# Kernel optimization log

Hardware: AMD Instinct MI355X
Metric: run time of the kernel (lower is better)

## Reference

```python
import jax, jax.numpy as jnp
import numpy as np

H = 8  # heads
EPS = 1e-5


def adaln(x, t, W, b):
    # AdaLayerNorm: emb = Linear(t); scale, shift = chunk(emb, 2, dim=-1)
    emb = t @ W + b                      # [B,1,2*D]
    scale, shift = jnp.split(emb, 2, axis=-1)
    mu = jnp.mean(x, axis=-1, keepdims=True)
    var = jnp.var(x, axis=-1, keepdims=True)
    xn = (x - mu) / jnp.sqrt(var + EPS)  # elementwise_affine=False
    return xn * (1.0 + scale) + shift


def attention(x, ctx, Wq, Wk, Wv, Wo, bo):
    B, N, D = x.shape
    d = D // H
    q = (x @ Wq).reshape(B, N, H, d).transpose(0, 2, 1, 3)          # [B,H,N,d]
    k = (ctx @ Wk).reshape(B, ctx.shape[1], H, d).transpose(0, 2, 1, 3)
    v = (ctx @ Wv).reshape(B, ctx.shape[1], H, d).transpose(0, 2, 1, 3)
    sim = jnp.einsum('bhid,bhjd->bhij', q, k) * (d ** -0.5)
    attn = jax.nn.softmax(sim, axis=-1)
    out = jnp.einsum('bhij,bhjd->bhid', attn, v)
    out = out.transpose(0, 2, 1, 3).reshape(B, N, D)
    return out @ Wo + bo


def geglu_ff(x, W1, b1, W2, b2):
    u, g = jnp.split(x @ W1 + b1, 2, axis=-1)
    return (u * jax.nn.gelu(g, approximate=False)) @ W2 + b2


def setup_inputs() -> dict:
    key = jax.random.key(0)
    ks = jax.random.split(key, 16)
    D = 512
    s = 0.02
    inp = {
        'x': jax.random.normal(ks[0], (2, 2048, D), jnp.float32),
        't': jax.random.normal(ks[1], (2, 1, D), jnp.float32),
        'cond': jax.random.normal(ks[2], (2, 1024, D), jnp.float32),
        'n1_w': jax.random.normal(ks[3], (D, 2 * D), jnp.float32) * s,
        'n1_b': jnp.zeros((2 * D,), jnp.float32),
        'n2_w': jax.random.normal(ks[4], (D, 2 * D), jnp.float32) * s,
        'n2_b': jnp.zeros((2 * D,), jnp.float32),
        'n4_w': jax.random.normal(ks[5], (D, 2 * D), jnp.float32) * s,
        'n4_b': jnp.zeros((2 * D,), jnp.float32),
        'a1_q': jax.random.normal(ks[6], (D, D), jnp.float32) * s,
        'a1_k': jax.random.normal(ks[7], (D, D), jnp.float32) * s,
        'a1_v': jax.random.normal(ks[8], (D, D), jnp.float32) * s,
        'a1_o': jax.random.normal(ks[9], (D, D), jnp.float32) * s,
        'a1_ob': jnp.zeros((D,), jnp.float32),
        'a2_q': jax.random.normal(ks[10], (D, D), jnp.float32) * s,
        'a2_k': jax.random.normal(ks[11], (D, D), jnp.float32) * s,
        'a2_v': jax.random.normal(ks[12], (D, D), jnp.float32) * s,
        'a2_o': jax.random.normal(ks[13], (D, D), jnp.float32) * s,
        'a2_ob': jnp.zeros((D,), jnp.float32),
        'ff_w1': jax.random.normal(ks[14], (D, 8 * D), jnp.float32) * s,
        'ff_b1': jnp.zeros((8 * D,), jnp.float32),
        'ff_w2': jax.random.normal(ks[15], (4 * D, D), jnp.float32) * s,
        'ff_b2': jnp.zeros((D,), jnp.float32),
    }
    return inp


def reference(x, t, cond, n1_w, n1_b, n2_w, n2_b, n4_w, n4_b,
              a1_q, a1_k, a1_v, a1_o, a1_ob,
              a2_q, a2_k, a2_v, a2_o, a2_ob,
              ff_w1, ff_b1, ff_w2, ff_b2):
    # BasicTransformerBlock, is_deform=False, withT=False, inference (dropout/droppath = identity, LayerScale = identity since init_values=0)
    h = adaln(x, t, n1_w, n1_b)
    x = attention(h, h, a1_q, a1_k, a1_v, a1_o, a1_ob) + x
    h = adaln(x, t, n2_w, n2_b)
    x = attention(h, cond, a2_q, a2_k, a2_v, a2_o, a2_ob) + x
    h = adaln(x, t, n4_w, n4_b)
    x = geglu_ff(h, ff_w1, ff_b1, ff_w2, ff_b2) + x
    return x
```

## Files before the change

### kernel.cpp

```cpp
#include <hip/hip_runtime.h>
#include <math.h>

#define D_MODEL 512
#define NHEADS  8
#define DHEAD   64

typedef __bf16  bf16x2 __attribute__((ext_vector_type(2)));
typedef __bf16  bf16x4 __attribute__((ext_vector_type(4)));
typedef __bf16  bf16x8 __attribute__((ext_vector_type(8)));
typedef float   f32x4  __attribute__((ext_vector_type(4)));

#define QSCALE 0.18033688f
#define DEFER_THR 11.5416f

__device__ __forceinline__ void gload16(const __bf16* g, __bf16* l) {
    __builtin_amdgcn_global_load_lds(
        (const __attribute__((address_space(1))) unsigned int*)g,
        (__attribute__((address_space(3))) unsigned int*)l, 16, 0, 0);
}

__device__ __forceinline__ void transpose_tile(
        const float* __restrict__ src, __bf16* __restrict__ dst,
        int K, int N, int k0, int n0) {
    __shared__ float t[64][65];
    int tid = threadIdx.x;
    int r = tid >> 6, c = tid & 63;
#pragma unroll
    for (int i = 0; i < 16; ++i)
        t[r + 4 * i][c] = src[(size_t)(k0 + r + 4 * i) * N + n0 + c];
    __syncthreads();
#pragma unroll
    for (int i = 0; i < 16; ++i)
        dst[(size_t)(n0 + r + 4 * i) * K + k0 + c] = (__bf16)t[c][r + 4 * i];
}

struct PrepArgs {
    const float *t, *n1w, *n1b, *n2w, *n2b, *n4w, *n4b;
    float* emb;
    const float* ws[8]; __bf16* wd[8];
    const float *ffw1, *ffw2;
    __bf16 *ff1t, *ff2t;
    const float* cond; __bf16* cbf;
    int B, condN;
};

__global__ __launch_bounds__(256) void prep_kernel(PrepArgs a) {
    int bb = blockIdx.x, tid = threadIdx.x;
    if (bb < 24) {
        int gI = bb * 256 + tid;
        int per = a.B * 2 * D_MODEL;
        if (gI >= 3 * per) return;
        int norm = gI / per;
        int rem  = gI - norm * per;
        int b = rem / (2 * D_MODEL);
        int c = rem % (2 * D_MODEL);
        const float* W  = (norm == 0) ? a.n1w : (norm == 1 ? a.n2w : a.n4w);
        const float* bb_= (norm == 0) ? a.n1b : (norm == 1 ? a.n2b : a.n4b);
        const float* trow = a.t + (size_t)b * D_MODEL;
        float acc = bb_[c];
        for (int k = 0; k < D_MODEL; ++k)
            acc = fmaf(trow[k], W[(size_t)k * (2 * D_MODEL) + c], acc);
        a.emb[gI] = acc;
    } else if (bb < 536) {
        int w = (bb - 24) >> 6, tI = (bb - 24) & 63;
        transpose_tile(a.ws[w], a.wd[w], 512, 512, (tI >> 3) << 6, (tI & 7) << 6);
    } else if (bb < 1048) {
        int tI = bb - 536;
        transpose_tile(a.ffw1, a.ff1t, 512, 4096, (tI & 7) << 6, (tI >> 3) << 6);
    } else if (bb < 1304) {
        int tI = bb - 1048;
        transpose_tile(a.ffw2, a.ff2t, 2048, 512, (tI >> 3) << 6, (tI & 7) << 6);
    } else {
        int i = ((bb - 1304) * 256 + tid) * 4;
        if (i >= a.condN) return;
        float4 v = *(const float4*)(a.cond + i);
        bf16x2 p0, p1;
        p0[0] = (__bf16)v.x; p0[1] = (__bf16)v.y;
        p1[0] = (__bf16)v.z; p1[1] = (__bf16)v.w;
        *(bf16x2*)(a.cbf + i)     = p0;
        *(bf16x2*)(a.cbf + i + 2) = p1;
    }
}

__global__ __launch_bounds__(256) void adaln_apply_kernel(
        const float* __restrict__ x, const float* __restrict__ emb_n,
        __bf16* __restrict__ h, int N) {
    int row = blockIdx.x;
    int b = row / N;
    const float* xr = x + (size_t)row * D_MODEL;
    int tid = threadIdx.x;
    float2 v = *(const float2*)(xr + 2 * tid);
    float s = v.x + v.y, sq = v.x * v.x + v.y * v.y;
#pragma unroll
    for (int off = 32; off; off >>= 1) {
        s  += __shfl_xor(s, off);
        sq += __shfl_xor(sq, off);
    }
    __shared__ float rs[4], rq[4];
    if ((tid & 63) == 0) { rs[tid >> 6] = s; rq[tid >> 6] = sq; }
    __syncthreads();
    float tot  = rs[0] + rs[1] + rs[2] + rs[3];
    float totq = rq[0] + rq[1] + rq[2] + rq[3];
    float mu  = tot * (1.0f / D_MODEL);
    float var = totq * (1.0f / D_MODEL) - mu * mu;
    float inv = rsqrtf(var + 1e-5f);
    const float* er = emb_n + (size_t)b * (2 * D_MODEL);
    float2 sc = *(const float2*)(er + 2 * tid);
    float2 sh = *(const float2*)(er + D_MODEL + 2 * tid);
    bf16x2 o;
    o[0] = (__bf16)((v.x - mu) * inv * (1.0f + sc.x) + sh.x);
    o[1] = (__bf16)((v.y - mu) * inv * (1.0f + sc.y) + sh.y);
    *(bf16x2*)(h + (size_t)row * D_MODEL + 2 * tid) = o;
}

template<int OUT, int WM>
__device__ __forceinline__ void gemm_body(
        const __bf16* __restrict__ A, const __bf16* __restrict__ Bt,
        const float* __restrict__ bias, const float* __restrict__ res,
        void* __restrict__ Cv, int M, int K, int N, int bx, int by,
        __bf16* As, __bf16* Bs) {
    constexpr int MI = WM / 16;
    int tid = threadIdx.x;
    int wave = tid >> 6, lane = tid & 63;
    int wr = wave >> 1, wc = wave & 1;
    int r = lane & 15, g = lane >> 4;
    int rx = r & 7;
    int m0 = by * (2 * WM), n0 = bx << 6;

    int lrow = lane >> 3;
    int lcol = ((lane & 7) ^ lrow) << 3;
    const __bf16* Ag = A  + (size_t)(m0 + (wave << 3) + lrow) * K + lcol;
    const __bf16* Bg = Bt + (size_t)(n0 + (wave << 3) + lrow) * K + lcol;
    __bf16* AsW = As + (size_t)(wave << 3) * 64;
    __bf16* BsW = Bs + (size_t)(wave << 3) * 64;

    f32x4 acc[MI][2];
#pragma unroll
    for (int mi = 0; mi < MI; ++mi)
#pragma unroll
        for (int ni = 0; ni < 2; ++ni) acc[mi][ni] = (f32x4){0.f, 0.f, 0.f, 0.f};

    for (int k0 = 0; k0 < K; k0 += 64) {
        if (k0) __syncthreads();
#pragma unroll
        for (int i = 0; i < MI; ++i)
            gload16(Ag + (size_t)(i * 32) * K + k0, AsW + i * 32 * 64);
#pragma unroll
        for (int j = 0; j < 2; ++j)
            gload16(Bg + (size_t)(j * 32) * K + k0, BsW + j * 32 * 64);
        __syncthreads();
#pragma unroll
        for (int kk = 0; kk < 2; ++kk) {
            int cs = ((((kk << 2) + g) ^ rx) << 3);
            bf16x8 af[MI], bf_[2];
#pragma unroll
            for (int mi = 0; mi < MI; ++mi)
                af[mi] = *(const bf16x8*)&As[(size_t)(wr * WM + (mi << 4) + r) * 64 + cs];
#pragma unroll
            for (int ni = 0; ni < 2; ++ni)
                bf_[ni] = *(const bf16x8*)&Bs[(size_t)((wc << 5) + (ni << 4) + r) * 64 + cs];
#pragma unroll
            for (int mi = 0; mi < MI; ++mi)
#pragma unroll
                for (int ni = 0; ni < 2; ++ni)
                    acc[mi][ni] = __builtin_amdgcn_mfma_f32_16x16x32_bf16(
                        af[mi], bf_[ni], acc[mi][ni], 0, 0, 0);
        }
    }

#pragma unroll
    for (int mi = 0; mi < MI; ++mi) {
#pragma unroll
        for (int ni = 0; ni < 2; ++ni) {
            int col = n0 + (wc << 5) + (ni << 4) + r;
            float scl = (OUT == 2 && col < 512) ? QSCALE : 1.0f;
#pragma unroll
            for (int rg = 0; rg < 4; ++rg) {
                int row = m0 + wr * WM + (mi << 4) + (g << 2) + rg;
                if (OUT == 1) {
                    float v = acc[mi][ni][rg] + bias[col] + res[(size_t)row * N + col];
                    ((float*)Cv)[(size_t)row * N + col] = v;
                } else {
                    ((__bf16*)Cv)[(size_t)row * N + col] = (__bf16)(acc[mi][ni][rg] * scl);
                }
            }
        }
    }
}

template<int OUT, int WM>
__global__ __launch_bounds__(256) void gemm_bf16_kernel(
        const __bf16* __restrict__ A, const __bf16* __restrict__ Bt,
        const float* __restrict__ bias, const float* __restrict__ res,
        void* __restrict__ Cv, int M, int K, int N) {
    __shared__ __attribute__((aligned(16))) __bf16 As[2 * WM * 64];
    __shared__ __attribute__((aligned(16))) __bf16 Bs[64 * 64];
    gemm_body<OUT, WM>(A, Bt, bias, res, Cv, M, K, N, blockIdx.x, blockIdx.y, As, Bs);
}

__global__ __launch_bounds__(256) void gemm_dual_kernel(
        const __bf16* A0, const __bf16* B0, __bf16* C0, int M0,
        const __bf16* A1, const __bf16* B1, __bf16* C1, int M1) {
    __shared__ __attribute__((aligned(16))) __bf16 As[64 * 64];
    __shared__ __attribute__((aligned(16))) __bf16 Bs[64 * 64];
    int nb0 = 8 * (M0 >> 6);
    if ((int)blockIdx.x < nb0) {
        gemm_body<2, 32>(A0, B0, nullptr, nullptr, C0, M0, 512, 512,
                         blockIdx.x & 7, blockIdx.x >> 3, As, Bs);
    } else {
        int id = blockIdx.x - nb0;
        gemm_body<0, 32>(A1, B1, nullptr, nullptr, C1, M1, 512, 1024,
                         id & 15, id >> 4, As, Bs);
    }
}

__global__ __launch_bounds__(256) void gemm_geglu_bf16_kernel(
        const __bf16* __restrict__ A, const __bf16* __restrict__ W1t,
        const float* __restrict__ b1, __bf16* __restrict__ gg, int M, int K) {
    const int NOUT = 4 * D_MODEL;
    __shared__ __attribute__((aligned(16))) __bf16 AsL[128 * 64];
    __shared__ __attribute__((aligned(16))) __bf16 BuL[64 * 64];
    __shared__ __attribute__((aligned(16))) __bf16 BgL[64 * 64];
    int tid = threadIdx.x;
    int wave = tid >> 6, lane = tid & 63;
    int wr = wave >> 1, wc = wave & 1;
    int r = lane & 15, g = lane >> 4;
    int rx = r & 7;
    int m0 = blockIdx.y << 7, n0 = blockIdx.x << 6;

    int lrow = lane >> 3;
    int lcol = ((lane & 7) ^ lrow) << 3;
    const __bf16* Ag = A   + (size_t)(m0 + (wave << 3) + lrow) * K + lcol;
    const __bf16* Ug = W1t + (size_t)(n0 + (wave << 3) + lrow) * K + lcol;
    const __bf16* Gg = W1t + (size_t)(NOUT + n0 + (wave << 3) + lrow) * K + lcol;
    __bf16* AsW = AsL + (size_t)(wave << 3) * 64;
    __bf16* BuW = BuL + (size_t)(wave << 3) * 64;
    __bf16* BgW = BgL + (size_t)(wave << 3) * 64;

    f32x4 accu[4][2], accg[4][2];
#pragma unroll
    for (int mi = 0; mi < 4; ++mi)
#pragma unroll
        for (int ni = 0; ni < 2; ++ni) {
            accu[mi][ni] = (f32x4){0.f, 0.f, 0.f, 0.f};
            accg[mi][ni] = (f32x4){0.f, 0.f, 0.f, 0.f};
        }

    for (int k0 = 0; k0 < K; k0 += 64) {
        if (k0) __syncthreads();
#pragma unroll
        for (int i = 0; i < 4; ++i)
            gload16(Ag + (size_t)(i * 32) * K + k0, AsW + i * 32 * 64);
#pragma unroll
        for (int j = 0; j < 2; ++j) {
            gload16(Ug + (size_t)(j * 32) * K + k0, BuW + j * 32 * 64);
            gload16(Gg + (size_t)(j * 32) * K + k0, BgW + j * 32 * 64);
        }
        __syncthreads();
#pragma unroll
        for (int kk = 0; kk < 2; ++kk) {
            int cs = ((((kk << 2) + g) ^ rx) << 3);
            bf16x8 af[4], bu[2], bg[2];
#pragma unroll
            for (int mi = 0; mi < 4; ++mi)
                af[mi] = *(const bf16x8*)&AsL[(size_t)((wr << 6) + (mi << 4) + r) * 64 + cs];
#pragma unroll
            for (int ni = 0; ni < 2; ++ni) {
                bu[ni] = *(const bf16x8*)&BuL[(size_t)((wc << 5) + (ni << 4) + r) * 64 + cs];
                bg[ni] = *(const bf16x8*)&BgL[(size_t)((wc << 5) + (ni << 4) + r) * 64 + cs];
            }
#pragma unroll
            for (int mi = 0; mi < 4; ++mi)
#pragma unroll
                for (int ni = 0; ni < 2; ++ni) {
                    accu[mi][ni] = __builtin_amdgcn_mfma_f32_16x16x32_bf16(
                        af[mi], bu[ni], accu[mi][ni], 0, 0, 0);
                    accg[mi][ni] = __builtin_amdgcn_mfma_f32_16x16x32_bf16(
                        af[mi], bg[ni], accg[mi][ni], 0, 0, 0);
                }
        }
    }

#pragma unroll
    for (int mi = 0; mi < 4; ++mi) {
#pragma unroll
        for (int ni = 0; ni < 2; ++ni) {
            int col = n0 + (wc << 5) + (ni << 4) + r;
            float bu_ = b1[col], bg_ = b1[NOUT + col];
#pragma unroll
            for (int rg = 0; rg < 4; ++rg) {
                int row = m0 + (wr << 6) + (mi << 4) + (g << 2) + rg;
                float u  = accu[mi][ni][rg] + bu_;
                float gv = accg[mi][ni][rg] + bg_;
                float ge = 0.5f * gv * (1.0f + erff(gv * 0.70710678118654752f));
                gg[(size_t)row * NOUT + col] = (__bf16)(u * ge);
            }
        }
    }
}

__global__ __launch_bounds__(512) void attn_mfma_kernel(
        const __bf16* __restrict__ q, const __bf16* __restrict__ k,
        const __bf16* __restrict__ v, __bf16* __restrict__ o,
        int Nq, int Nk, int sq, int skv) {
    __shared__ __attribute__((aligned(16))) __bf16 Ks[2][4096];
    __shared__ __attribute__((aligned(16))) __bf16 Vt[2][4096];
    __shared__ __attribute__((aligned(16))) __bf16 Pl[8][1024];

    int tid = threadIdx.x;
    int w = tid >> 6, lane = tid & 63;
    int r = lane & 15, g = lane >> 4;
    int rx = r & 7;

    int nqb = Nq >> 7;
    int qb = blockIdx.x % nqb;
    int hh = (blockIdx.x / nqb) % NHEADS;
    int b  = blockIdx.x / (nqb * NHEADS);

    const __bf16* qp = q + ((size_t)(b * Nq + (qb << 7) + (w << 4) + r)) * sq
                         + hh * DHEAD + (g << 3);
    bf16x8 qf0 = *(const bf16x8*)qp;
    bf16x8 qf1 = *(const bf16x8*)(qp + 32);

    bool isK = (tid >= 256);
    int sidx = tid & 255;
    int krow = sidx >> 2, kp_ = sidx & 3;
    int va = sidx & 31, vbb = sidx >> 5;
    size_t kvbase = (size_t)b * Nk * skv + (size_t)hh * DHEAD;
    const __bf16* kp = k + kvbase + (size_t)krow * skv + (kp_ << 4);
    const __bf16* vp = v + kvbase + (size_t)(2 * va) * skv + (vbb << 3);
    int kwo0 = krow * 64 + ((((kp_ << 1) | 0) ^ (krow & 7)) << 3);
    int kwo1 = krow * 64 + ((((kp_ << 1) | 1) ^ (krow & 7)) << 3);
    int vwb  = vbb * 512 + ((va & 3) << 1);

    f32x4 oacc[4];
#pragma unroll
    for (int dt = 0; dt < 4; ++dt) oacc[dt] = (f32x4){0.f, 0.f, 0.f, 0.f};
    float m = -1e30f, l = 0.f;
    f32x4 saccA[4], saccB[4];
    bf16x8 sr0, sr1;
    bf16x8 vf[2][4], pa[2];

    auto LOADREG = [&](int t) {
        if (isK) {
            const __bf16* kp2 = kp + (size_t)t * 64 * skv;
            sr0 = *(const bf16x8*)kp2; sr1 = *(const bf16x8*)(kp2 + 8);
        } else {
            const __bf16* vp2 = vp + (size_t)t * 64 * skv;
            sr0 = *(const bf16x8*)vp2; sr1 = *(const bf16x8*)(vp2 + skv);
        }
    };
    auto STAGEW = [&](int buf) {
        if (isK) {
            *(bf16x8*)&Ks[buf][kwo0] = sr0;
            *(bf16x8*)&Ks[buf][kwo1] = sr1;
        } else {
#pragma unroll
            for (int j = 0; j < 8; ++j) {
                bf16x2 pr; pr[0] = sr0[j]; pr[1] = sr1[j];
                *(bf16x2*)&Vt[buf][vwb + j * 64 + (((va >> 2) ^ j) << 3)] = pr;
            }
        }
    };
    auto QKT = [&](f32x4 (&sacc)[4], int buf) {
#pragma unroll
        for (int nt = 0; nt < 4; ++nt) sacc[nt] = (f32x4){0.f, 0.f, 0.f, 0.f};
        __builtin_amdgcn_s_setprio(1);
#pragma unroll
        for (int nt = 0; nt < 4; ++nt) {
            bf16x8 kf0 = *(const bf16x8*)&Ks[buf][((nt << 4) + r) * 64 + ((g ^ rx) << 3)];
            bf16x8 kf1 = *(const bf16x8*)&Ks[buf][((nt << 4) + r) * 64 + (((g + 4) ^ rx) << 3)];
            sacc[nt] = __builtin_amdgcn_mfma_f32_16x16x32_bf16(kf0, qf0, sacc[nt], 0, 0, 0);
            sacc[nt] = __builtin_amdgcn_mfma_f32_16x16x32_bf16(kf1, qf1, sacc[nt], 0, 0, 0);
        }
        __builtin_amdgcn_s_setprio(0);
    };
    auto SMAX = [&](f32x4 (&sacc)[4]) {
        float mx = sacc[0][0];
#pragma unroll
        for (int nt = 0; nt < 4; ++nt)
#pragma unroll
            for (int rg = 0; rg < 4; ++rg) mx = fmaxf(mx, sacc[nt][rg]);
        mx = fmaxf(mx, __shfl_xor(mx, 16));
        mx = fmaxf(mx, __shfl_xor(mx, 32));
        if (!__all(mx <= m + DEFER_THR)) {
            float mn = fmaxf(m, mx);
            float al = exp2f(m - mn);
            m = mn; l *= al;
#pragma unroll
            for (int dt = 0; dt < 4; ++dt)
#pragma unroll
                for (int rg = 0; rg < 4; ++rg) oacc[dt][rg] *= al;
        }
        float sum = 0.f;
#pragma unroll
        for (int nt = 0; nt < 4; ++nt) {
            bf16x4 pk;
#pragma unroll
            for (int rg = 0; rg < 4; ++rg) {
                float p = exp2f(sacc[nt][rg] - m);
                sum += p;
                pk[rg] = (__bf16)p;
            }
            *(bf16x4*)&Pl[w][r * 64 + ((((nt << 1) | (g >> 1)) ^ rx) << 3) + ((g & 1) << 2)] = pk;
        }
        l += sum;
    };
    auto VFLOAD = [&](int buf) {
#pragma unroll
        for (int kh = 0; kh < 2; ++kh) {
            pa[kh] = *(const bf16x8*)&Pl[w][r * 64 + ((((kh << 2) + g) ^ rx) << 3)];
#pragma unroll
            for (int dt = 0; dt < 4; ++dt)
                vf[kh][dt] = *(const bf16x8*)&Vt[buf][((dt << 4) + r) * 64
                                                      + ((((kh << 2) + g) ^ rx) << 3)];
        }
    };
    auto PVOP = [&]() {
        __builtin_amdgcn_s_setprio(1);
#pragma unroll
        for (int kh = 0; kh < 2; ++kh)
#pragma unroll
            for (int dt = 0; dt < 4; ++dt)
                oacc[dt] = __builtin_amdgcn_mfma_f32_16x16x32_bf16(
                    vf[kh][dt], pa[kh], oacc[dt], 0, 0, 0);
        __builtin_amdgcn_s_setprio(0);
    };

    int ntiles = Nk >> 6;
    LOADREG(0);
    STAGEW(0);
    LOADREG(1);
    __syncthreads();
    QKT(saccA, 0);

    for (int t = 0; t + 1 < ntiles; t += 2) {
        STAGEW(1);
        if (t + 2 < ntiles) LOADREG(t + 2);
        SMAX(saccA);
        VFLOAD(0);
        __syncthreads();
        QKT(saccB, 1);
        PVOP();
        if (t + 2 < ntiles) {
            STAGEW(0);
            if (t + 3 < ntiles) LOADREG(t + 3);
        }
        SMAX(saccB);
        VFLOAD(1);
        __syncthreads();
        if (t + 2 < ntiles) QKT(saccA, 0);
        PVOP();
    }

    l += __shfl_xor(l, 16);
    l += __shfl_xor(l, 32);
    float inv = 1.0f / l;
    __bf16* ob = o + ((size_t)(b * Nq + (qb << 7) + (w << 4) + r)) * D_MODEL + hh * DHEAD;
#pragma unroll
    for (int dt = 0; dt < 4; ++dt) {
        bf16x4 ov;
#pragma unroll
        for (int rg = 0; rg < 4; ++rg) ov[rg] = (__bf16)(oacc[dt][rg] * inv);
        *(bf16x4*)&ob[(dt << 4) + (g << 2)] = ov;
    }
}

extern "C" void kernel_launch(void* const* d_in, const int* in_sizes, int n_in,
                              void* d_out, int out_size, void* d_ws, size_t ws_size,
                              hipStream_t stream) {
    const float* x    = (const float*)d_in[0];
    const float* t    = (const float*)d_in[1];
    const float* cond = (const float*)d_in[2];
    const float* n1_w = (const float*)d_in[3];
    const float* n1_b = (const float*)d_in[4];
    const float* n2_w = (const float*)d_in[5];
    const float* n2_b = (const float*)d_in[6];
    const float* n4_w = (const float*)d_in[7];
    const float* n4_b = (const float*)d_in[8];
    const float* a1_q = (const float*)d_in[9];
    const float* a1_k = (const float*)d_in[10];
    const float* a1_v = (const float*)d_in[11];
    const float* a1_o = (const float*)d_in[12];
    const float* a1_ob= (const float*)d_in[13];
    const float* a2_q = (const float*)d_in[14];
    const float* a2_k = (const float*)d_in[15];
    const float* a2_v = (const float*)d_in[16];
    const float* a2_o = (const float*)d_in[17];
    const float* a2_ob= (const float*)d_in[18];
    const float* ff_w1= (const float*)d_in[19];
    const float* ff_b1= (const float*)d_in[20];
    const float* ff_w2= (const float*)d_in[21];
    const float* ff_b2= (const float*)d_in[22];
    float* out = (float*)d_out;

    const int B  = in_sizes[1] / D_MODEL;
    const int N  = in_sizes[0] / (B * D_MODEL);
    const int Nc = in_sizes[2] / (B * D_MODEL);
    const int R  = B * N;
    const int Rc = B * Nc;

    char* Wb = (char*)d_ws;
    float* emb   = (float*)Wb;
    __bf16* r1   = (__bf16*)(Wb + 32768);
    __bf16* qkv  = r1;
    __bf16* q2   = r1;
    __bf16* kv2  = r1 + (size_t)R * 512;
    __bf16* gg   = r1;
    __bf16* h_bf = (__bf16*)(Wb + 32768 + 16777216);
    __bf16* c_bf = (__bf16*)(Wb + 32768 + 16777216 + 4194304);
    __bf16* wts  = (__bf16*)(Wb + 32768 + 16777216 + 4194304 + 2097152);
    __bf16* a1_qt = wts;
    __bf16* a1_ot = wts + 3 * 262144;
    __bf16* a2_qt = wts + 4 * 262144;
    __bf16* a2_kt = wts + 5 * 262144;
    __bf16* a2_ot = wts + 7 * 262144;
    __bf16* ff1t  = wts + 8 * 262144;
    __bf16* ff2t  = ff1t + 2097152;

    dim3 blk(256);

    PrepArgs pa;
    pa.t = t; pa.n1w = n1_w; pa.n1b = n1_b; pa.n2w = n2_w; pa.n2b = n2_b;
    pa.n4w = n4_w; pa.n4b = n4_b; pa.emb = emb;
    pa.ws[0] = a1_q; pa.ws[1] = a1_k; pa.ws[2] = a1_v; pa.ws[3] = a1_o;
    pa.ws[4] = a2_q; pa.ws[5] = a2_k; pa.ws[6] = a2_v; pa.ws[7] = a2_o;
    pa.wd[0] = a1_qt; pa.wd[1] = wts + 262144; pa.wd[2] = wts + 2 * 262144; pa.wd[3] = a1_ot;
    pa.wd[4] = a2_qt; pa.wd[5] = a2_kt; pa.wd[6] = wts + 6 * 262144; pa.wd[7] = a2_ot;
    pa.ffw1 = ff_w1; pa.ffw2 = ff_w2; pa.ff1t = ff1t; pa.ff2t = ff2t;
    pa.cond = cond; pa.cbf = c_bf; pa.B = B; pa.condN = Rc * D_MODEL;
    prep_kernel<<<dim3(1304 + (Rc * D_MODEL) / 1024), blk, 0, stream>>>(pa);

    adaln_apply_kernel<<<dim3(R), blk, 0, stream>>>(x, emb, h_bf, N);
    gemm_bf16_kernel<2, 64><<<dim3(24, R / 128), blk, 0, stream>>>(
        h_bf, a1_qt, nullptr, nullptr, qkv, R, 512, 1536);
    attn_mfma_kernel<<<dim3(B * NHEADS * (N / 128)), dim3(512), 0, stream>>>(
        qkv, qkv + 512, qkv + 1024, h_bf, N, N, 1536, 1536);
    gemm_bf16_kernel<1, 32><<<dim3(8, R / 64), blk, 0, stream>>>(
        h_bf, a1_ot, a1_ob, x, out, R, 512, 512);

    adaln_apply_kernel<<<dim3(R), blk, 0, stream>>>(
        out, emb + (size_t)B * 2 * D_MODEL, h_bf, N);
    gemm_dual_kernel<<<dim3(8 * (R / 64) + 16 * (Rc / 64)), blk, 0, stream>>>(
        h_bf, a2_qt, q2, R, c_bf, a2_kt, kv2, Rc);
    attn_mfma_kernel<<<dim3(B * NHEADS * (N / 128)), dim3(512), 0, stream>>>(
        q2, kv2, kv2 + 512, h_bf, N, Nc, 512, 1024);
    gemm_bf16_kernel<1, 32><<<dim3(8, R / 64), blk, 0, stream>>>(
        h_bf, a2_ot, a2_ob, out, out, R, 512, 512);

    adaln_apply_kernel<<<dim3(R), blk, 0, stream>>>(
        out, emb + (size_t)2 * B * 2 * D_MODEL, h_bf, N);
    gemm_geglu_bf16_kernel<<<dim3(32, R / 128), blk, 0, stream>>>(
        h_bf, ff1t, ff_b1, gg, R, 512);
    gemm_bf16_kernel<1, 32><<<dim3(8, R / 64), blk, 0, stream>>>(
        gg, ff2t, ff_b2, out, out, R, 2048, 512);
}
```

Baseline: 211.3 us.

## Split attention KV range across two blocks and merge partials

```diff
diff --git a/kernel.cpp b/kernel.cpp
--- a/kernel.cpp
+++ b/kernel.cpp
@@ -301,7 +301,8 @@
 
 __global__ __launch_bounds__(512) void attn_mfma_kernel(
         const __bf16* __restrict__ q, const __bf16* __restrict__ k,
-        const __bf16* __restrict__ v, __bf16* __restrict__ o,
+        const __bf16* __restrict__ v, __bf16* __restrict__ op0,
+        __bf16* __restrict__ op1, float* __restrict__ ml,
         int Nq, int Nk, int sq, int skv) {
     __shared__ __attribute__((aligned(16))) __bf16 Ks[2][4096];
     __shared__ __attribute__((aligned(16))) __bf16 Vt[2][4096];
@@ -312,6 +313,9 @@
     int r = lane & 15, g = lane >> 4;
     int rx = r & 7;
 
+    int split = blockIdx.y;
+    int kvlen = Nk >> 1;
+
     int nqb = Nq >> 7;
     int qb = blockIdx.x % nqb;
     int hh = (blockIdx.x / nqb) % NHEADS;
@@ -326,7 +330,8 @@
     int sidx = tid & 255;
     int krow = sidx >> 2, kp_ = sidx & 3;
     int va = sidx & 31, vbb = sidx >> 5;
-    size_t kvbase = (size_t)b * Nk * skv + (size_t)hh * DHEAD;
+    size_t kvbase = (size_t)b * Nk * skv + (size_t)hh * DHEAD
+                  + (size_t)split * kvlen * skv;
     const __bf16* kp = k + kvbase + (size_t)krow * skv + (kp_ << 4);
     const __bf16* vp = v + kvbase + (size_t)(2 * va) * skv + (vbb << 3);
     int kwo0 = krow * 64 + ((((kp_ << 1) | 0) ^ (krow & 7)) << 3);
@@ -427,7 +432,7 @@
         __builtin_amdgcn_s_setprio(0);
     };
 
-    int ntiles = Nk >> 6;
+    int ntiles = kvlen >> 6;
     LOADREG(0);
     STAGEW(0);
     LOADREG(1);
@@ -455,15 +460,44 @@
 
     l += __shfl_xor(l, 16);
     l += __shfl_xor(l, 32);
-    float inv = 1.0f / l;
-    __bf16* ob = o + ((size_t)(b * Nq + (qb << 7) + (w << 4) + r)) * D_MODEL + hh * DHEAD;
+    int rowq = (qb << 7) + (w << 4) + r;
+    __bf16* ob = (split ? op1 : op0)
+               + ((size_t)(b * Nq + rowq)) * D_MODEL + hh * DHEAD;
 #pragma unroll
     for (int dt = 0; dt < 4; ++dt) {
         bf16x4 ov;
 #pragma unroll
-        for (int rg = 0; rg < 4; ++rg) ov[rg] = (__bf16)(oacc[dt][rg] * inv);
+        for (int rg = 0; rg < 4; ++rg) ov[rg] = (__bf16)oacc[dt][rg];
         *(bf16x4*)&ob[(dt << 4) + (g << 2)] = ov;
     }
+    if (g == 0) {
+        size_t mi_ = ((((size_t)(b * NHEADS + hh) * Nq + rowq) << 1) + split) << 1;
+        ml[mi_]     = m;
+        ml[mi_ + 1] = l;
+    }
+}
+
+__global__ __launch_bounds__(256) void attn_merge_kernel(
+        const __bf16* __restrict__ p0, const __bf16* __restrict__ p1,
+        const float* __restrict__ ml, __bf16* __restrict__ out, int Nq) {
+    int i = blockIdx.x * 256 + threadIdx.x;
+    int oct = i & 63, rowg = i >> 6;
+    int b = rowg / Nq, row = rowg - b * Nq;
+    int h = oct >> 3;
+    size_t mb = (((size_t)(b * NHEADS + h) * Nq + row) << 2);
+    float m0 = ml[mb], l0 = ml[mb + 1], m1 = ml[mb + 2], l1 = ml[mb + 3];
+    float mm = fmaxf(m0, m1);
+    float a0 = exp2f(m0 - mm), a1 = exp2f(m1 - mm);
+    float inv = 1.0f / (a0 * l0 + a1 * l1);
+    a0 *= inv; a1 *= inv;
+    size_t off = (size_t)rowg * D_MODEL + oct * 8;
+    bf16x8 x0 = *(const bf16x8*)(p0 + off);
+    bf16x8 x1 = *(const bf16x8*)(p1 + off);
+    bf16x8 o;
+#pragma unroll
+    for (int j = 0; j < 8; ++j)
+        o[j] = (__bf16)(a0 * (float)x0[j] + a1 * (float)x1[j]);
+    *(bf16x8*)(out + off) = o;
 }
 
 extern "C" void kernel_launch(void* const* d_in, const int* in_sizes, int n_in,
@@ -507,6 +541,9 @@
     __bf16* q2   = r1;
     __bf16* kv2  = r1 + (size_t)R * 512;
     __bf16* gg   = r1;
+    __bf16* p0s  = r1 + (size_t)R * 1536;
+    __bf16* p0c  = r1 + (size_t)4 * 1048576;
+    __bf16* p1c  = r1 + (size_t)6 * 1048576;
     __bf16* h_bf = (__bf16*)(Wb + 32768 + 16777216);
     __bf16* c_bf = (__bf16*)(Wb + 32768 + 16777216 + 4194304);
     __bf16* wts  = (__bf16*)(Wb + 32768 + 16777216 + 4194304 + 2097152);
@@ -517,6 +554,7 @@
     __bf16* a2_ot = wts + 7 * 262144;
     __bf16* ff1t  = wts + 8 * 262144;
     __bf16* ff2t  = ff1t + 2097152;
+    float* mlbuf = (float*)(Wb + 32768 + 16777216 + 4194304 + 2097152 + 10485760);
 
     dim3 blk(256);
 
@@ -534,8 +572,10 @@
     adaln_apply_kernel<<<dim3(R), blk, 0, stream>>>(x, emb, h_bf, N);
     gemm_bf16_kernel<2, 64><<<dim3(24, R / 128), blk, 0, stream>>>(
         h_bf, a1_qt, nullptr, nullptr, qkv, R, 512, 1536);
-    attn_mfma_kernel<<<dim3(B * NHEADS * (N / 128)), dim3(512), 0, stream>>>(
-        qkv, qkv + 512, qkv + 1024, h_bf, N, N, 1536, 1536);
+    attn_mfma_kernel<<<dim3(B * NHEADS * (N / 128), 2), dim3(512), 0, stream>>>(
+        qkv, qkv + 512, qkv + 1024, p0s, h_bf, mlbuf, N, N, 1536, 1536);
+    attn_merge_kernel<<<dim3(R * 64 / 256), blk, 0, stream>>>(
+        p0s, h_bf, mlbuf, h_bf, N);
     gemm_bf16_kernel<1, 32><<<dim3(8, R / 64), blk, 0, stream>>>(
         h_bf, a1_ot, a1_ob, x, out, R, 512, 512);
 
@@ -543,8 +583,10 @@
         out, emb + (size_t)B * 2 * D_MODEL, h_bf, N);
     gemm_dual_kernel<<<dim3(8 * (R / 64) + 16 * (Rc / 64)), blk, 0, stream>>>(
         h_bf, a2_qt, q2, R, c_bf, a2_kt, kv2, Rc);
-    attn_mfma_kernel<<<dim3(B * NHEADS * (N / 128)), dim3(512), 0, stream>>>(
-        q2, kv2, kv2 + 512, h_bf, N, Nc, 512, 1024);
+    attn_mfma_kernel<<<dim3(B * NHEADS * (N / 128), 2), dim3(512), 0, stream>>>(
+        q2, kv2, kv2 + 512, p0c, p1c, mlbuf, N, Nc, 512, 1024);
+    attn_merge_kernel<<<dim3(R * 64 / 256), blk, 0, stream>>>(
+        p0c, p1c, mlbuf, h_bf, N);
     gemm_bf16_kernel<1, 32><<<dim3(8, R / 64), blk, 0, stream>>>(
         h_bf, a2_ot, a2_ob, out, out, R, 512, 512);
 
```

New measurement: 224.9 us. 1.06x slower.
